# Kernel tuning notes

Hardware: AMD Instinct MI355X
Metric: run time of the kernel (lower is better)

## Reference

```python
import jax, jax.numpy as jnp
import numpy as np

HIDDEN = 1024
HEADS = 8
HEAD = HIDDEN // HEADS
EPS = 1e-5


def _gammas():
    lo = np.log(1.0 / 512.0)
    hi = np.log(1.0 / 32.0)
    lin = np.linspace(lo, hi, HEADS)
    return jnp.asarray(1.0 - np.exp(lin), dtype=jnp.float32)  # [H]


def setup_inputs() -> dict:
    key = jax.random.key(0)
    ks = jax.random.split(key, 7)
    B, S = 2, 2048
    x = jax.random.normal(ks[0], (B, S, HIDDEN), dtype=jnp.float32)
    # Per-head retention projection weights (Retention(head_size, gamma)): [H, d, d]
    Wq = jax.random.normal(ks[1], (HEADS, HEAD, HEAD), dtype=jnp.float32) / HEAD
    Wk = jax.random.normal(ks[2], (HEADS, HEAD, HEAD), dtype=jnp.float32) / HEAD
    Wv = jax.random.normal(ks[3], (HEADS, HEAD, HEAD), dtype=jnp.float32) / HEAD
    W1 = jax.random.normal(ks[4], (HIDDEN, HIDDEN), dtype=jnp.float32) / HIDDEN
    W2 = jax.random.normal(ks[5], (HIDDEN, HIDDEN), dtype=jnp.float32) / HIDDEN
    gn_w = jnp.ones((HIDDEN,), dtype=jnp.float32)
    gn_b = jnp.zeros((HIDDEN,), dtype=jnp.float32)
    return {"x": x, "Wq": Wq, "Wk": Wk, "Wv": Wv, "W1": W1, "W2": W2,
            "gn_w": gn_w, "gn_b": gn_b}


def _decay_mask(S, gammas):
    idx = jnp.arange(S)
    diff = idx[:, None] - idx[None, :]              # [S, S]
    causal = diff >= 0
    safe = jnp.where(causal, diff, 0).astype(jnp.float32)
    D = jnp.where(causal[None], gammas[:, None, None] ** safe[None], 0.0)  # [H,S,S]
    return D


def _msr_forward(x, Wq, Wk, Wv, W1, W2, gn_w, gn_b):
    B, S, _ = x.shape
    xh = x.reshape(B, S, HEADS, HEAD)               # per-head slices
    q = jnp.einsum('bshd,hde->bshe', xh, Wq)
    k = jnp.einsum('bshd,hde->bshe', xh, Wk)
    v = jnp.einsum('bshd,hde->bshe', xh, Wv)
    D = _decay_mask(S, _gammas())                   # [H,S,S]
    scores = jnp.einsum('bnhd,bmhd->bhnm', q, k) * D[None]
    ret = jnp.einsum('bhnm,bmhd->bnhd', scores, v)  # [B,S,H,d]
    # GroupNorm(num_groups=H, channels=HIDDEN) over flattened rows
    mu = jnp.mean(ret, axis=-1, keepdims=True)
    var = jnp.var(ret, axis=-1, keepdims=True)
    ret = (ret - mu) * jax.lax.rsqrt(var + EPS)
    ret = ret.reshape(B, S, HIDDEN) * gn_w + gn_b
    gated = x @ W1
    out = gated * jax.nn.sigmoid(gated) + ret       # swish gate + residual add
    return out @ W2


def reference(x, Wq, Wk, Wv, W1, W2, gn_w, gn_b):
    return _msr_forward(x, Wq, Wk, Wv, W1, W2, gn_w, gn_b)
```

## Files before the change

### kernel.cpp

```cpp
#include <hip/hip_runtime.h>
#include <hip/hip_bf16.h>

#define HID 1024
#define NH 8
#define HD 128
#define BB 2
#define SS 2048
#define CHK 128
#define NCH 16

typedef __attribute__((ext_vector_type(8))) short short8;
typedef __attribute__((ext_vector_type(4))) float f32x4;

static __device__ __forceinline__ float b2f(unsigned short u){
  unsigned int x = ((unsigned int)u) << 16; float f;
  __builtin_memcpy(&f, &x, 4); return f;
}
static __device__ __forceinline__ unsigned short f2b(float f){
  unsigned int x; __builtin_memcpy(&x, &f, 4);
  x += 0x7fffu + ((x >> 16) & 1u);
  return (unsigned short)(x >> 16);
}
static __device__ __forceinline__ float head_gamma(int h){
  double lo = -6.238324625039508;
  double hi = -3.4657359027997265;
  double lin = lo + (hi - lo) * ((double)h / 7.0);
  return (float)(1.0 - exp(lin));
}
static __device__ __forceinline__ f32x4 MFMA(short8 a, short8 b, f32x4 c){
  return __builtin_amdgcn_mfma_f32_16x16x32_bf16(a, b, c, 0, 0, 0);
}

typedef const __attribute__((address_space(1))) unsigned int* gas1_u32p;
typedef __attribute__((address_space(3))) unsigned int* las3_u32p;
static __device__ __forceinline__ void gload_lds16(const void* g, void* l){
  __builtin_amdgcn_global_load_lds((gas1_u32p)g, (las3_u32p)l, 16, 0, 0);
}

__global__ __launch_bounds__(256) void k_prep(
    const float* __restrict__ x,  unsigned short* __restrict__ xb,
    const float* __restrict__ W1, unsigned short* __restrict__ w1T,
    const float* __restrict__ W2, unsigned short* __restrict__ w2T,
    const float* __restrict__ Wq, unsigned short* __restrict__ wqT,
    const float* __restrict__ Wk, unsigned short* __restrict__ wkT,
    const float* __restrict__ Wv, unsigned short* __restrict__ wvT)
{
  int bid = blockIdx.x, t = threadIdx.x;
  if (bid < 1024){
    const int n = BB*SS*HID;
    int i = (bid*256 + t)*4;
    const int st = 1024*256*4;
    for (; i < n; i += st){
      float4 v = *(const float4*)(x + i);
      unsigned short o[4] = { f2b(v.x), f2b(v.y), f2b(v.z), f2b(v.w) };
      *(uint2*)(xb + i) = *(const uint2*)o;
    }
    return;
  }
  __shared__ float tile[32][33];
  const float* in; unsigned short* out; int R, C, r0, c0;
  if (bid < 3072){
    int which = (bid - 1024) >> 10;
    int local = (bid - 1024) & 1023;
    in  = which ? W2 : W1;  out = which ? w2T : w1T;
    R = C = HID;
    c0 = (local & 31)*32; r0 = (local >> 5)*32;
  } else {
    int local = bid - 3072;
    int mat = local >> 7;
    int rem = local & 127;
    int z = rem >> 4, tl2 = rem & 15;
    const float* ws[3] = { Wq, Wk, Wv };
    unsigned short* os[3] = { wqT, wkT, wvT };
    in  = ws[mat] + (size_t)z*HD*HD;
    out = os[mat] + (size_t)z*HD*HD;
    R = C = HD;
    c0 = (tl2 & 3)*32; r0 = (tl2 >> 2)*32;
  }
  int tx = t & 31, ty = t >> 5;
  #pragma unroll
  for (int i=0;i<4;i++) tile[ty+i*8][tx] = in[(size_t)(r0+ty+i*8)*C + c0+tx];
  __syncthreads();
  #pragma unroll
  for (int i=0;i<4;i++) out[(size_t)(c0+ty+i*8)*R + r0+tx] = f2b(tile[tx][ty+i*8]);
}

__global__ __launch_bounds__(256) void k_qkv(
    const unsigned short* __restrict__ xb,
    const unsigned short* __restrict__ wqT,
    const unsigned short* __restrict__ wkT,
    const unsigned short* __restrict__ wvT,
    unsigned short* __restrict__ qb,
    unsigned short* __restrict__ kb,
    unsigned short* __restrict__ ktsb,
    unsigned short* __restrict__ vtb)
{
  int bid = blockIdx.x;
  int stile = bid & 31;
  int bh = bid >> 5;
  int h = bh & 7, b = bh >> 3;
  int T0 = stile*64;
  int chunk = stile >> 1, pm0 = (stile & 1)*64;
  float l2g = log2f(head_gamma(h));
  __shared__ unsigned short tl[128*72];
  int t = threadIdx.x, wv = t>>6, l = t&63, lr = l&15, lg = l>>4;
  int row0 = T0 + wv*16;
  short8 a[4];
  const unsigned short* xp = xb + (size_t)(b*SS + row0 + lr)*HID + h*HD + lg*8;
  #pragma unroll
  for (int kk=0;kk<4;kk++) a[kk] = *(const short8*)(xp + kk*32);
  size_t obase = ((size_t)bh*SS + row0)*HD;
  size_t tbase = ((size_t)(bh*NCH + chunk))*HD*CHK + pm0;

  auto wout = [&](unsigned short* dst){
    int e = t & 127, th = t >> 7;
    const uint4* src = (const uint4*)(tl + e*72 + th*32);
    uint4* d4 = (uint4*)(dst + (size_t)e*CHK + th*32);
    #pragma unroll
    for (int i=0;i<4;i++) d4[i] = src[i];
  };

  {
    const unsigned short* wb = wqT + (size_t)h*HD*HD;
    unsigned short* op = qb + obase;
    #pragma unroll
    for (int nt=0;nt<8;nt++){
      f32x4 acc = {0.f,0.f,0.f,0.f};
      #pragma unroll
      for (int kk=0;kk<4;kk++){
        short8 bfr = *(const short8*)(wb + (size_t)(nt*16+lr)*HD + kk*32 + lg*8);
        acc = MFMA(a[kk], bfr, acc);
      }
      #pragma unroll
      for (int r=0;r<4;r++)
        op[(size_t)(lg*4+r)*HD + nt*16 + lr] = f2b(acc[r]);
    }
  }
  {
    const unsigned short* wb = wkT + (size_t)h*HD*HD;
    unsigned short* op = kb + obase;
    float ksc[4];
    #pragma unroll
    for (int r=0;r<4;r++)
      ksc[r] = exp2f((float)(127 - (pm0 + wv*16 + lg*4 + r))*l2g);
    #pragma unroll
    for (int nt=0;nt<8;nt++){
      f32x4 acc = {0.f,0.f,0.f,0.f};
      #pragma unroll
      for (int kk=0;kk<4;kk++){
        short8 bfr = *(const short8*)(wb + (size_t)(nt*16+lr)*HD + kk*32 + lg*8);
        acc = MFMA(a[kk], bfr, acc);
      }
      #pragma unroll
      for (int r=0;r<4;r++){
        op[(size_t)(lg*4+r)*HD + nt*16 + lr] = f2b(acc[r]);
        tl[(nt*16+lr)*72 + wv*16 + lg*4 + r] = f2b(acc[r]*ksc[r]);
      }
    }
  }
  __syncthreads();
  wout(ktsb + tbase);
  __syncthreads();
  {
    const unsigned short* wb = wvT + (size_t)h*HD*HD;
    #pragma unroll
    for (int nt=0;nt<8;nt++){
      f32x4 acc = {0.f,0.f,0.f,0.f};
      #pragma unroll
      for (int kk=0;kk<4;kk++){
        short8 bfr = *(const short8*)(wb + (size_t)(nt*16+lr)*HD + kk*32 + lg*8);
        acc = MFMA(a[kk], bfr, acc);
      }
      #pragma unroll
      for (int r=0;r<4;r++)
        tl[(nt*16+lr)*72 + wv*16 + lg*4 + r] = f2b(acc[r]);
    }
  }
  __syncthreads();
  wout(vtb + tbase);
}

__global__ __launch_bounds__(256) void k_sumscan(
    const unsigned short* __restrict__ ktsb,
    const unsigned short* __restrict__ vtb,
    unsigned short* __restrict__ ST)
{
  int bid = blockIdx.x;
  int dh = bid & 1, et = (bid >> 1) & 7, bh = bid >> 4;
  int h = bh & 7;
  float d128 = exp2f(128.f * log2f(head_gamma(h)));
  int t = threadIdx.x, wv = t>>6, l = t&63, lr = l&15, lg = l>>4;
  int e0 = et*16;
  int d0w = dh*64 + wv*16;
  const unsigned short* vt = vtb  + (size_t)bh*NCH*HD*CHK;
  const unsigned short* kt = ktsb + (size_t)bh*NCH*HD*CHK;
  unsigned short* Sb = ST + (size_t)bh*NCH*HD*HD;

  f32x4 s = {0.f,0.f,0.f,0.f};
  #pragma unroll
  for (int c=0;c<NCH;c++){
    const unsigned short* vc = vt + (size_t)c*HD*CHK;
    const unsigned short* kc = kt + (size_t)c*HD*CHK;
    f32x4 acc = {0.f,0.f,0.f,0.f};
    #pragma unroll
    for (int kk=0;kk<4;kk++){
      short8 af = *(const short8*)(vc + (size_t)(e0+lr)*CHK + kk*32 + lg*8);
      short8 bf = *(const short8*)(kc + (size_t)(d0w+lr)*CHK + kk*32 + lg*8);
      acc = MFMA(af, bf, acc);
    }
    unsigned short* So = Sb + (size_t)c*HD*HD;
    #pragma unroll
    for (int r=0;r<4;r++){
      So[(size_t)(e0+lg*4+r)*HD + d0w + lr] = f2b(s[r]);
      s[r] = s[r]*d128 + acc[r];
    }
  }
}

__global__ __launch_bounds__(512) void k_g1ret(
    const unsigned short* __restrict__ A,
    const unsigned short* __restrict__ BT,
    const unsigned short* __restrict__ qb,
    const unsigned short* __restrict__ kb,
    const unsigned short* __restrict__ vtb,
    const unsigned short* __restrict__ ST,
    const float* __restrict__ gnw,
    const float* __restrict__ gnb,
    unsigned short* __restrict__ Cb,
    int M, int N, int K)
{
  __shared__ unsigned short lsu[65536];
  const int nb = N >> 7;
  const int nwg = (M >> 7) * nb;
  const int cpx = nwg >> 3;
  int bid0 = blockIdx.x;
  int bid = (bid0 & 7)*cpx + (bid0 >> 3);
  const int m0 = (bid / nb) << 7;
  const int n0 = (bid % nb) << 7;
  const int t = threadIdx.x, wv = t>>6, l = t&63, lr = l&15, lg = l>>4;
  const int wr = (wv>>1)<<5;
  const int wc = (wv&1)<<6;
  const int srow = l >> 3;
  const int sgc  = ((l & 7) ^ srow) << 3;
  const unsigned short* Abase = A  + (size_t)(m0 + wv*16 + srow)*K + sgc;
  const unsigned short* Bbase = BT + (size_t)(n0 + wv*16 + srow)*K + sgc;

  auto stage = [&](int buf, int kt){
    unsigned short* la = lsu + buf*16384;
    unsigned short* lb = la + 8192;
    int k0 = kt << 6;
    #pragma unroll
    for (int it=0; it<2; ++it){
      gload_lds16(Abase + (size_t)(it*8)*K + k0, la + (wv*16 + it*8)*64);
      gload_lds16(Bbase + (size_t)(it*8)*K + k0, lb + (wv*16 + it*8)*64);
    }
  };
  auto stageMat = [&](const unsigned short* g, int reg){
    #pragma unroll
    for (int i=0;i<4;i++){
      int c = i*512 + t;
      int row = c >> 4, p = c & 15;
      gload_lds16(g + row*128 + ((p ^ (row & 7)) << 3),
                  lsu + reg + (i*512 + (t & 448))*8);
    }
  };

  const int b = m0 >> 11, j = (m0 >> 7) & 15, h = n0 >> 7;
  const int bh = b*NH + h;
  const int cj = bh*NCH + j;
  float l2g = log2f(head_gamma(h));
  const unsigned short* qc = qb + ((size_t)bh*SS + j*CHK)*HD;
  const unsigned short* kc = kb + ((size_t)bh*SS + j*CHK)*HD;
  const unsigned short* vt = vtb + (size_t)cj*HD*CHK;
  const unsigned short* Sp = ST + (size_t)cj*HD*HD;

  short8 qf[4];
  #pragma unroll
  for (int kk=0;kk<4;kk++)
    qf[kk] = *(const short8*)(qc + (size_t)(wv*16 + lr)*HD + kk*32 + lg*8);

  f32x4 acc[2][4];
  #pragma unroll
  for (int i=0;i<2;i++)
    #pragma unroll
    for (int j2=0;j2<4;j2++) acc[i][j2] = (f32x4){0,0,0,0};

  const int NT = K >> 6;
  stage(0,0); stage(1,1); stage(2,2);
  for (int kt = 0; kt < NT; ++kt){
    if (kt < NT-2)       asm volatile("s_waitcnt vmcnt(8)" ::: "memory");
    else if (kt == NT-2) asm volatile("s_waitcnt vmcnt(4)" ::: "memory");
    else                 asm volatile("s_waitcnt vmcnt(0)" ::: "memory");
    __builtin_amdgcn_s_barrier();
    __builtin_amdgcn_sched_barrier(0);
    if (kt+3 < NT) stage((kt+3)&3, kt+3);
    if (kt == NT-3) stageMat(Sp, 0);
    if (kt == NT-2) stageMat(vt, 16384);
    if (kt == NT-1) stageMat(kc, 32768);
    const unsigned short* pa = lsu + (kt&3)*16384;
    const unsigned short* pb = pa + 8192;
    #pragma unroll
    for (int ks=0; ks<2; ++ks){
      short8 af[2], bf[4];
      #pragma unroll
      for (int i=0;i<2;i++){
        int ra = wr + i*16 + lr;
        af[i] = *(const short8*)(pa + ra*64 + ((((ks<<2)+lg) ^ (ra&7))<<3));
      }
      #pragma unroll
      for (int j2=0;j2<4;j2++){
        int rb = wc + j2*16 + lr;
        bf[j2] = *(const short8*)(pb + rb*64 + ((((ks<<2)+lg) ^ (rb&7))<<3));
      }
      #pragma unroll
      for (int i=0;i<2;i++)
        #pragma unroll
        for (int j2=0;j2<4;j2++)
          acc[i][j2] = MFMA(af[i], bf[j2], acc[i][j2]);
    }
  }
  __syncthreads();

  f32x4 racc[8];
  #pragma unroll
  for (int nt=0;nt<8;nt++){
    f32x4 aa = {0,0,0,0};
    #pragma unroll
    for (int kk=0;kk<4;kk++){
      short8 bfr = *(const short8*)(lsu + (nt*16+lr)*128 + (((kk*4+lg) ^ (lr&7))<<3));
      aa = MFMA(qf[kk], bfr, aa);
    }
    racc[nt] = aa;
  }
  #pragma unroll
  for (int r=0;r<4;r++){
    int n = wv*16 + lg*4 + r;
    float sf = exp2f((float)(n+1)*l2g);
    #pragma unroll
    for (int nt=0;nt<8;nt++) racc[nt][r] *= sf;
  }
  __syncthreads();

  int ntmax = (wv | 1) + 1;
  for (int nt=0; nt<ntmax; nt++){
    f32x4 a0 = {0,0,0,0};
    #pragma unroll
    for (int kk=0;kk<4;kk++){
      short8 bfr = *(const short8*)(lsu + 32768 + (nt*16+lr)*128 + (((kk*4+lg) ^ (lr&7))<<3));
      a0 = MFMA(qf[kk], bfr, a0);
    }
    int col = nt*16 + lr;
    #pragma unroll
    for (int r=0;r<4;r++){
      int lrow = wv*16 + lg*4 + r;
      float v0 = (col <= lrow) ? a0[r]*exp2f((float)(lrow-col)*l2g) : 0.f;
      lsu[lrow*128 + (((col>>3) ^ (lrow&7))<<3) + (col&7)] = f2b(v0);
    }
  }

  #pragma unroll
  for (int i=0;i<2;i++){
    #pragma unroll
    for (int j2=0;j2<4;j2++){
      #pragma unroll
      for (int r=0;r<4;r++){
        int row = wr + i*16 + lg*4 + r;
        int col = wc + j2*16 + lr;
        float v = acc[i][j2][r];
        lsu[49152 + row*128 + (((col>>3) ^ (row&7))<<3) + (col&7)]
          = f2b(v / (1.f + __expf(-v)));
      }
    }
  }

  int ksmax = (wv >> 1) + 1;
  for (int ks=0; ks<ksmax; ks++){
    short8 afr = *(const short8*)(lsu + (wv*16+lr)*128 + (((ks*4+lg) ^ (lr&7))<<3));
    #pragma unroll
    for (int nt=0;nt<8;nt++){
      short8 bfr = *(const short8*)(lsu + 16384 + (nt*16+lr)*128 + (((ks*4+lg) ^ (lr&7))<<3));
      racc[nt] = MFMA(afr, bfr, racc[nt]);
    }
  }
  __syncthreads();

  unsigned short* op = Cb + (size_t)(m0 + wv*16)*N + n0;
  const float* gw  = gnw + h*HD;
  const float* gbb = gnb + h*HD;
  #pragma unroll
  for (int r=0;r<4;r++){
    float s = 0.f, ss = 0.f;
    #pragma unroll
    for (int nt=0;nt<8;nt++){ float x = racc[nt][r]; s += x; ss += x*x; }
    #pragma unroll
    for (int off=1; off<16; off<<=1){
      s  += __shfl_xor(s,  off, 64);
      ss += __shfl_xor(ss, off, 64);
    }
    float mu  = s*(1.f/128.f);
    float var = ss*(1.f/128.f) - mu*mu;
    float rs  = rsqrtf(var + 1e-5f);
    int lrow = lg*4 + r;
    int Rr = wv*16 + lrow;
    unsigned short* orow = op + (size_t)lrow*N;
    #pragma unroll
    for (int nt=0;nt<8;nt++){
      int col = nt*16 + lr;
      float rv = (racc[nt][r]-mu)*rs*gw[col] + gbb[col];
      float cv = b2f(lsu[49152 + Rr*128 + (((col>>3) ^ (Rr&7))<<3) + (col&7)]);
      orow[col] = f2b(rv + cv);
    }
  }
}

__global__ __launch_bounds__(512) void k_gemm2(
    const unsigned short* __restrict__ A,
    const unsigned short* __restrict__ BT,
    float* __restrict__ Cf,
    int M, int N, int K)
{
  __shared__ unsigned short ls[4][2][128*64];
  const int nb = N >> 7;
  const int nwg = (M >> 7) * nb;
  const int cpx = nwg >> 3;
  int bid0 = blockIdx.x;
  int bid = (bid0 & 7)*cpx + (bid0 >> 3);
  const int m0 = (bid / nb) << 7;
  const int n0 = (bid % nb) << 7;
  const int t = threadIdx.x, wv = t>>6, l = t&63, lr = l&15, lg = l>>4;
  const int wr = (wv>>1)<<5;
  const int wc = (wv&1)<<6;
  const int srow = l >> 3;
  const int sgc  = ((l & 7) ^ srow) << 3;
  const unsigned short* Abase = A  + (size_t)(m0 + wv*16 + srow)*K + sgc;
  const unsigned short* Bbase = BT + (size_t)(n0 + wv*16 + srow)*K + sgc;

  auto stage = [&](int buf, int kt){
    unsigned short* la = &ls[buf][0][0];
    unsigned short* lb = &ls[buf][1][0];
    int k0 = kt << 6;
    #pragma unroll
    for (int it=0; it<2; ++it){
      gload_lds16(Abase + (size_t)(it*8)*K + k0, la + (wv*16 + it*8)*64);
      gload_lds16(Bbase + (size_t)(it*8)*K + k0, lb + (wv*16 + it*8)*64);
    }
  };

  f32x4 acc[2][4];
  #pragma unroll
  for (int i=0;i<2;i++)
    #pragma unroll
    for (int j=0;j<4;j++) acc[i][j] = (f32x4){0,0,0,0};

  const int NT = K >> 6;
  stage(0,0); stage(1,1); stage(2,2);
  for (int kt = 0; kt < NT; ++kt){
    if (kt < NT-2)       asm volatile("s_waitcnt vmcnt(8)" ::: "memory");
    else if (kt == NT-2) asm volatile("s_waitcnt vmcnt(4)" ::: "memory");
    else                 asm volatile("s_waitcnt vmcnt(0)" ::: "memory");
    __builtin_amdgcn_s_barrier();
    __builtin_amdgcn_sched_barrier(0);
    if (kt+3 < NT) stage((kt+3)&3, kt+3);
    const unsigned short* pa = &ls[kt&3][0][0];
    const unsigned short* pb = &ls[kt&3][1][0];
    #pragma unroll
    for (int ks=0; ks<2; ++ks){
      short8 af[2], bf[4];
      #pragma unroll
      for (int i=0;i<2;i++){
        int ra = wr + i*16 + lr;
        af[i] = *(const short8*)(pa + ra*64 + ((((ks<<2)+lg) ^ (ra&7))<<3));
      }
      #pragma unroll
      for (int j=0;j<4;j++){
        int rb = wc + j*16 + lr;
        bf[j] = *(const short8*)(pb + rb*64 + ((((ks<<2)+lg) ^ (rb&7))<<3));
      }
      #pragma unroll
      for (int i=0;i<2;i++)
        #pragma unroll
        for (int j=0;j<4;j++)
          acc[i][j] = MFMA(af[i], bf[j], acc[i][j]);
    }
  }

  #pragma unroll
  for (int i=0;i<2;i++)
    #pragma unroll
    for (int j=0;j<4;j++)
      #pragma unroll
      for (int r=0;r<4;r++){
        int row = m0 + wr + i*16 + lg*4 + r;
        int col = n0 + wc + j*16 + lr;
        Cf[(size_t)row*N + col] = acc[i][j][r];
      }
}

extern "C" void kernel_launch(void* const* d_in, const int* in_sizes, int n_in,
                              void* d_out, int out_size, void* d_ws, size_t ws_size,
                              hipStream_t stream)
{
  (void)in_sizes; (void)n_in; (void)out_size; (void)ws_size;
  const float* x   = (const float*)d_in[0];
  const float* Wq  = (const float*)d_in[1];
  const float* Wk  = (const float*)d_in[2];
  const float* Wv  = (const float*)d_in[3];
  const float* W1  = (const float*)d_in[4];
  const float* W2  = (const float*)d_in[5];
  const float* gnw = (const float*)d_in[6];
  const float* gnb = (const float*)d_in[7];
  float* out = (float*)d_out;

  char* wsp = (char*)d_ws;
  size_t off = 0;
  auto alloc = [&](size_t bytes)->void*{
    off = (off + 255) & ~(size_t)255;
    void* p = wsp + off; off += bytes; return p;
  };
  const size_t NTOK = (size_t)BB*SS;
  unsigned short* xb   = (unsigned short*)alloc(NTOK*HID*2);
  unsigned short* w1T  = (unsigned short*)alloc((size_t)HID*HID*2);
  unsigned short* w2T  = (unsigned short*)alloc((size_t)HID*HID*2);
  unsigned short* wqT  = (unsigned short*)alloc((size_t)NH*HD*HD*2);
  unsigned short* wkT  = (unsigned short*)alloc((size_t)NH*HD*HD*2);
  unsigned short* wvT  = (unsigned short*)alloc((size_t)NH*HD*HD*2);
  unsigned short* qb   = (unsigned short*)alloc(NTOK*HID*2);
  unsigned short* kb   = (unsigned short*)alloc(NTOK*HID*2);
  unsigned short* ktsb = (unsigned short*)alloc(NTOK*HID*2);
  unsigned short* vtb  = (unsigned short*)alloc(NTOK*HID*2);
  unsigned short* ST   = (unsigned short*)alloc((size_t)BB*NH*NCH*HD*HD*2);
  unsigned short* opb  = (unsigned short*)alloc(NTOK*HID*2);

  k_prep<<<dim3(3456), dim3(256), 0, stream>>>(x, xb, W1, w1T, W2, w2T,
                                               Wq, wqT, Wk, wkT, Wv, wvT);
  k_qkv<<<dim3(BB*NH*32), dim3(256), 0, stream>>>(xb, wqT, wkT, wvT, qb, kb, ktsb, vtb);
  k_sumscan<<<dim3(BB*NH*16), dim3(256), 0, stream>>>(ktsb, vtb, ST);

  k_g1ret<<<dim3(256), dim3(512), 0, stream>>>(xb, w1T, qb, kb, vtb, ST, gnw, gnb,
                                               opb, (int)NTOK, HID, HID);
  k_gemm2<<<dim3(256), dim3(512), 0, stream>>>(opb, w2T, out, (int)NTOK, HID, HID);
}
```

Baseline: 100.2 us.

## Fuse x bf16 conversion into QKV kernel and stage g1ret output through LDS

The fp32-to-bf16 conversion of x moves out of the prep kernel and into the QKV projection kernel, which already loads each head slice of x. That kernel now converts while loading and also writes the bf16 copy for the later gate GEMM, saving one full read of x and a separate pass. The g1ret epilogue now writes its normalized results into swizzled LDS and then stores them to global as coalesced 16-byte rows instead of scattered 2-byte stores. The cost is an extra __syncthreads and the reuse of the LDS region.

```diff
diff --git a/kernel.cpp b/kernel.cpp
--- a/kernel.cpp
+++ b/kernel.cpp
@@ -38,7 +38,6 @@
 }
 
 __global__ __launch_bounds__(256) void k_prep(
-    const float* __restrict__ x,  unsigned short* __restrict__ xb,
     const float* __restrict__ W1, unsigned short* __restrict__ w1T,
     const float* __restrict__ W2, unsigned short* __restrict__ w2T,
     const float* __restrict__ Wq, unsigned short* __restrict__ wqT,
@@ -46,27 +45,16 @@
     const float* __restrict__ Wv, unsigned short* __restrict__ wvT)
 {
   int bid = blockIdx.x, t = threadIdx.x;
-  if (bid < 1024){
-    const int n = BB*SS*HID;
-    int i = (bid*256 + t)*4;
-    const int st = 1024*256*4;
-    for (; i < n; i += st){
-      float4 v = *(const float4*)(x + i);
-      unsigned short o[4] = { f2b(v.x), f2b(v.y), f2b(v.z), f2b(v.w) };
-      *(uint2*)(xb + i) = *(const uint2*)o;
-    }
-    return;
-  }
   __shared__ float tile[32][33];
   const float* in; unsigned short* out; int R, C, r0, c0;
-  if (bid < 3072){
-    int which = (bid - 1024) >> 10;
-    int local = (bid - 1024) & 1023;
+  if (bid < 2048){
+    int which = bid >> 10;
+    int local = bid & 1023;
     in  = which ? W2 : W1;  out = which ? w2T : w1T;
     R = C = HID;
     c0 = (local & 31)*32; r0 = (local >> 5)*32;
   } else {
-    int local = bid - 3072;
+    int local = bid - 2048;
     int mat = local >> 7;
     int rem = local & 127;
     int z = rem >> 4, tl2 = rem & 15;
@@ -86,10 +74,11 @@
 }
 
 __global__ __launch_bounds__(256) void k_qkv(
-    const unsigned short* __restrict__ xb,
+    const float* __restrict__ x,
     const unsigned short* __restrict__ wqT,
     const unsigned short* __restrict__ wkT,
     const unsigned short* __restrict__ wvT,
+    unsigned short* __restrict__ xb,
     unsigned short* __restrict__ qb,
     unsigned short* __restrict__ kb,
     unsigned short* __restrict__ ktsb,
@@ -106,9 +95,17 @@
   int t = threadIdx.x, wv = t>>6, l = t&63, lr = l&15, lg = l>>4;
   int row0 = T0 + wv*16;
   short8 a[4];
-  const unsigned short* xp = xb + (size_t)(b*SS + row0 + lr)*HID + h*HD + lg*8;
-  #pragma unroll
-  for (int kk=0;kk<4;kk++) a[kk] = *(const short8*)(xp + kk*32);
+  const float* xp = x + (size_t)(b*SS + row0 + lr)*HID + h*HD + lg*8;
+  unsigned short* xbw = xb + (size_t)(b*SS + row0 + lr)*HID + h*HD + lg*8;
+  #pragma unroll
+  for (int kk=0;kk<4;kk++){
+    float4 v0 = *(const float4*)(xp + kk*32);
+    float4 v1 = *(const float4*)(xp + kk*32 + 4);
+    unsigned short tmp[8] = { f2b(v0.x), f2b(v0.y), f2b(v0.z), f2b(v0.w),
+                              f2b(v1.x), f2b(v1.y), f2b(v1.z), f2b(v1.w) };
+    a[kk] = *(const short8*)tmp;
+    *(short8*)(xbw + kk*32) = a[kk];
+  }
   size_t obase = ((size_t)bh*SS + row0)*HD;
   size_t tbase = ((size_t)(bh*NCH + chunk))*HD*CHK + pm0;
 
@@ -384,14 +381,13 @@
   }
   __syncthreads();
 
-  unsigned short* op = Cb + (size_t)(m0 + wv*16)*N + n0;
   const float* gw  = gnw + h*HD;
   const float* gbb = gnb + h*HD;
   #pragma unroll
   for (int r=0;r<4;r++){
     float s = 0.f, ss = 0.f;
     #pragma unroll
-    for (int nt=0;nt<8;nt++){ float x = racc[nt][r]; s += x; ss += x*x; }
+    for (int nt=0;nt<8;nt++){ float x2 = racc[nt][r]; s += x2; ss += x2*x2; }
     #pragma unroll
     for (int off=1; off<16; off<<=1){
       s  += __shfl_xor(s,  off, 64);
@@ -400,15 +396,25 @@
     float mu  = s*(1.f/128.f);
     float var = ss*(1.f/128.f) - mu*mu;
     float rs  = rsqrtf(var + 1e-5f);
-    int lrow = lg*4 + r;
-    int Rr = wv*16 + lrow;
-    unsigned short* orow = op + (size_t)lrow*N;
+    int Rr = wv*16 + lg*4 + r;
     #pragma unroll
     for (int nt=0;nt<8;nt++){
       int col = nt*16 + lr;
       float rv = (racc[nt][r]-mu)*rs*gw[col] + gbb[col];
       float cv = b2f(lsu[49152 + Rr*128 + (((col>>3) ^ (Rr&7))<<3) + (col&7)]);
-      orow[col] = f2b(rv + cv);
+      lsu[Rr*128 + (((col>>3) ^ (Rr&7))<<3) + (col&7)] = f2b(rv + cv);
+    }
+  }
+  __syncthreads();
+
+  {
+    int row = t >> 2, cg = t & 3;
+    unsigned short* orow = Cb + (size_t)(m0 + row)*N + n0 + cg*32;
+    const unsigned short* lrp = lsu + row*128;
+    #pragma unroll
+    for (int i=0;i<4;i++){
+      int c0 = cg*32 + i*8;
+      *(uint4*)(orow + i*8) = *(const uint4*)(lrp + (((c0>>3) ^ (row&7))<<3));
     }
   }
 }
@@ -531,9 +537,9 @@
   unsigned short* ST   = (unsigned short*)alloc((size_t)BB*NH*NCH*HD*HD*2);
   unsigned short* opb  = (unsigned short*)alloc(NTOK*HID*2);
 
-  k_prep<<<dim3(3456), dim3(256), 0, stream>>>(x, xb, W1, w1T, W2, w2T,
+  k_prep<<<dim3(2432), dim3(256), 0, stream>>>(W1, w1T, W2, w2T,
                                                Wq, wqT, Wk, wkT, Wv, wvT);
-  k_qkv<<<dim3(BB*NH*32), dim3(256), 0, stream>>>(xb, wqT, wkT, wvT, qb, kb, ktsb, vtb);
+  k_qkv<<<dim3(BB*NH*32), dim3(256), 0, stream>>>(x, wqT, wkT, wvT, xb, qb, kb, ktsb, vtb);
   k_sumscan<<<dim3(BB*NH*16), dim3(256), 0, stream>>>(ktsb, vtb, ST);
 
   k_g1ret<<<dim3(256), dim3(512), 0, stream>>>(xb, w1T, qb, kb, vtb, ST, gnw, gnb,
```

Result: no change. 101.1 us (+0.9%).

## Load GEMM2 MFMA fragments directly from global memory instead of LDS staging

Applied to the files above, without the earlier changes.

The final output GEMM kernel no longer stages A and B tiles through a 4-deep LDS ring buffer with async global-to-LDS loads, waitcnt and barriers. Each wave now reads its MFMA operand fragments straight from global memory in 32-wide K steps, unrolled by 4. This removes LDS traffic, barriers and shared-memory occupancy limits, but gives up cross-wave reuse of tiles (each A/B row is fetched by multiple waves) and relies on L2/L1 caching and strided 16-byte loads.

```diff
diff --git a/kernel.cpp b/kernel.cpp
--- a/kernel.cpp
+++ b/kernel.cpp
@@ -419,7 +419,6 @@
     float* __restrict__ Cf,
     int M, int N, int K)
 {
-  __shared__ unsigned short ls[4][2][128*64];
   const int nb = N >> 7;
   const int nwg = (M >> 7) * nb;
   const int cpx = nwg >> 3;
@@ -430,21 +429,13 @@
   const int t = threadIdx.x, wv = t>>6, l = t&63, lr = l&15, lg = l>>4;
   const int wr = (wv>>1)<<5;
   const int wc = (wv&1)<<6;
-  const int srow = l >> 3;
-  const int sgc  = ((l & 7) ^ srow) << 3;
-  const unsigned short* Abase = A  + (size_t)(m0 + wv*16 + srow)*K + sgc;
-  const unsigned short* Bbase = BT + (size_t)(n0 + wv*16 + srow)*K + sgc;
-
-  auto stage = [&](int buf, int kt){
-    unsigned short* la = &ls[buf][0][0];
-    unsigned short* lb = &ls[buf][1][0];
-    int k0 = kt << 6;
-    #pragma unroll
-    for (int it=0; it<2; ++it){
-      gload_lds16(Abase + (size_t)(it*8)*K + k0, la + (wv*16 + it*8)*64);
-      gload_lds16(Bbase + (size_t)(it*8)*K + k0, lb + (wv*16 + it*8)*64);
-    }
-  };
+
+  const unsigned short* Ar0 = A  + (size_t)(m0 + wr      + lr)*K + lg*8;
+  const unsigned short* Ar1 = A  + (size_t)(m0 + wr + 16 + lr)*K + lg*8;
+  const unsigned short* Br0 = BT + (size_t)(n0 + wc      + lr)*K + lg*8;
+  const unsigned short* Br1 = BT + (size_t)(n0 + wc + 16 + lr)*K + lg*8;
+  const unsigned short* Br2 = BT + (size_t)(n0 + wc + 32 + lr)*K + lg*8;
+  const unsigned short* Br3 = BT + (size_t)(n0 + wc + 48 + lr)*K + lg*8;
 
   f32x4 acc[2][4];
   #pragma unroll
@@ -452,36 +443,22 @@
     #pragma unroll
     for (int j=0;j<4;j++) acc[i][j] = (f32x4){0,0,0,0};
 
-  const int NT = K >> 6;
-  stage(0,0); stage(1,1); stage(2,2);
-  for (int kt = 0; kt < NT; ++kt){
-    if (kt < NT-2)       asm volatile("s_waitcnt vmcnt(8)" ::: "memory");
-    else if (kt == NT-2) asm volatile("s_waitcnt vmcnt(4)" ::: "memory");
-    else                 asm volatile("s_waitcnt vmcnt(0)" ::: "memory");
-    __builtin_amdgcn_s_barrier();
-    __builtin_amdgcn_sched_barrier(0);
-    if (kt+3 < NT) stage((kt+3)&3, kt+3);
-    const unsigned short* pa = &ls[kt&3][0][0];
-    const unsigned short* pb = &ls[kt&3][1][0];
-    #pragma unroll
-    for (int ks=0; ks<2; ++ks){
-      short8 af[2], bf[4];
-      #pragma unroll
-      for (int i=0;i<2;i++){
-        int ra = wr + i*16 + lr;
-        af[i] = *(const short8*)(pa + ra*64 + ((((ks<<2)+lg) ^ (ra&7))<<3));
-      }
-      #pragma unroll
-      for (int j=0;j<4;j++){
-        int rb = wc + j*16 + lr;
-        bf[j] = *(const short8*)(pb + rb*64 + ((((ks<<2)+lg) ^ (rb&7))<<3));
-      }
-      #pragma unroll
-      for (int i=0;i<2;i++)
-        #pragma unroll
-        for (int j=0;j<4;j++)
-          acc[i][j] = MFMA(af[i], bf[j], acc[i][j]);
-    }
+  #pragma unroll 4
+  for (int kc = 0; kc < K; kc += 32){
+    short8 af0 = *(const short8*)(Ar0 + kc);
+    short8 af1 = *(const short8*)(Ar1 + kc);
+    short8 bf0 = *(const short8*)(Br0 + kc);
+    short8 bf1 = *(const short8*)(Br1 + kc);
+    short8 bf2 = *(const short8*)(Br2 + kc);
+    short8 bf3 = *(const short8*)(Br3 + kc);
+    acc[0][0] = MFMA(af0, bf0, acc[0][0]);
+    acc[0][1] = MFMA(af0, bf1, acc[0][1]);
+    acc[0][2] = MFMA(af0, bf2, acc[0][2]);
+    acc[0][3] = MFMA(af0, bf3, acc[0][3]);
+    acc[1][0] = MFMA(af1, bf0, acc[1][0]);
+    acc[1][1] = MFMA(af1, bf1, acc[1][1]);
+    acc[1][2] = MFMA(af1, bf2, acc[1][2]);
+    acc[1][3] = MFMA(af1, bf3, acc[1][3]);
   }
 
   #pragma unroll
```

Result: slower. 132.4 us (+32.1%).
